# Kernel tuning notes

Hardware: AMD Instinct MI355X
Metric: run time of the kernel (lower is better)

Reference implementation:

```python
import jax, jax.numpy as jnp
import numpy as np

B, C, H, W = 8, 128, 48, 48
RED = 16  # SELayer reduction


def setup_inputs() -> dict:
    key = jax.random.key(0)
    ks = jax.random.split(key, 8)
    s = 0.05  # weight scale for numerical stability of softmax
    return {
        "x": jax.random.normal(ks[0], (B, C, H, W), jnp.float32),
        "Wq": jax.random.normal(ks[1], (C, C), jnp.float32) * s,
        "bq": jnp.zeros((C,), jnp.float32),
        "Wk": jax.random.normal(ks[2], (C, C), jnp.float32) * s,
        "bk": jnp.zeros((C,), jnp.float32),
        "Wv": jax.random.normal(ks[3], (C, C), jnp.float32) * s,
        "bv": jnp.zeros((C,), jnp.float32),
        "se_w1": jax.random.normal(ks[4], (C // RED, C), jnp.float32) * s,
        "se_w2": jax.random.normal(ks[5], (C, C // RED), jnp.float32) * s,
        "gamma": jax.random.normal(ks[6], (1,), jnp.float32),
    }


def reference(x, Wq, bq, Wk, bk, Wv, bv, se_w1, se_w2, gamma):
    b, c, h, w = x.shape
    n = h * w
    xf = x.reshape(b, c, n)  # (B, C, N)
    # 1x1 convs == per-pixel linear maps over channels
    q = jnp.einsum('oc,bcn->bon', Wq, xf) + bq[None, :, None]  # (B, C, N)
    k = jnp.einsum('oc,bcn->bon', Wk, xf) + bk[None, :, None]
    v = jnp.einsum('oc,bcn->bon', Wv, xf) + bv[None, :, None]
    # energy[b, i, j] = sum_c q[b, c, i] * k[b, c, j]  (unscaled, as in source)
    energy = jnp.einsum('bci,bcj->bij', q, k)  # (B, N, N)
    attn = jax.nn.softmax(energy, axis=-1)
    # out[b, c, i] = sum_j v[b, c, j] * attn[b, i, j]
    out = jnp.einsum('bcj,bij->bci', v, attn).reshape(b, c, h, w)
    # SELayer applied to the input x
    y = jnp.mean(x, axis=(2, 3))  # (B, C) global average pool
    y = jax.nn.relu(y @ se_w1.T)  # (B, C//RED)
    y = jax.nn.sigmoid(y @ se_w2.T)  # (B, C)
    x_se = x * y[:, :, None, None]
    return gamma[0] * out + x_se
```

## Files before the change

kernel.cpp:

```cpp
#include <hip/hip_runtime.h>

typedef _Float16 half8 __attribute__((ext_vector_type(8)));
typedef _Float16 half4 __attribute__((ext_vector_type(4)));
typedef float f32x4 __attribute__((ext_vector_type(4)));

#define BATCH 8
#define CH 128
#define NPIX 2304
#define SPLIT 4
#define JPER (NPIX / SPLIT)
#define BN (BATCH * NPIX)
#define LOG2E 1.44269504088896f

__device__ __forceinline__ f32x4 mfma32(half8 a, half8 b, f32x4 c) {
    return __builtin_amdgcn_mfma_f32_16x16x32_f16(a, b, c, 0, 0, 0);
}
__device__ __forceinline__ f32x4 mfma16(half4 a, half4 b, f32x4 c) {
    return __builtin_amdgcn_mfma_f32_16x16x16f16(a, b, c, 0, 0, 0);
}

__global__ __launch_bounds__(256) void k_prep(
        const float* __restrict__ x, const float* __restrict__ Wq,
        const float* __restrict__ Wk, const float* __restrict__ Wv,
        _Float16* __restrict__ Wh, float* __restrict__ y0) {
    const int bid = blockIdx.x;
    const int t = threadIdx.x;
    if (bid < 1024) {
        const int row = bid;
        const float4* p = (const float4*)(x + (size_t)row * NPIX);
        float s = 0.f;
        for (int tt = t; tt < NPIX / 4; tt += 256) {
            float4 v = p[tt];
            s += v.x + v.y + v.z + v.w;
        }
        for (int m = 1; m < 64; m <<= 1) s += __shfl_xor(s, m);
        __shared__ float ls[4];
        if ((t & 63) == 0) ls[t >> 6] = s;
        __syncthreads();
        if (t == 0) y0[row] = (ls[0] + ls[1] + ls[2] + ls[3]) * (1.0f / (float)NPIX);
    } else {
        int i = (bid - 1024) * 256 + t;
        const float* src = (i < 16384) ? Wq : ((i < 32768) ? Wk : Wv);
        Wh[i] = (_Float16)src[i & 16383];
    }
}

__global__ __launch_bounds__(256) void k_proj(
        const float* __restrict__ x, const _Float16* __restrict__ Wh,
        const float* __restrict__ bq, const float* __restrict__ bk, const float* __restrict__ bv,
        _Float16* __restrict__ qT, _Float16* __restrict__ kT, _Float16* __restrict__ vN,
        const float* __restrict__ y0, const float* __restrict__ se_w1,
        const float* __restrict__ se_w2, float* __restrict__ scale) {
    const int which = blockIdx.z;
    const int t = threadIdx.x;

    if (which == 3) {
        if (blockIdx.x != 0 || blockIdx.y != 0) return;
        __shared__ float ly[128];
        __shared__ float ly1[8];
        for (int b = 0; b < BATCH; ++b) {
            if (t < 128) ly[t] = y0[b * 128 + t];
            __syncthreads();
            if (t < 8) {
                float a = 0.f;
                for (int c = 0; c < 128; ++c) a += se_w1[t * 128 + c] * ly[c];
                ly1[t] = fmaxf(a, 0.f);
            }
            __syncthreads();
            if (t < 128) {
                float a = 0.f;
                for (int r = 0; r < 8; ++r) a += se_w2[t * 8 + r] * ly1[r];
                scale[b * 128 + t] = 1.f / (1.f + __expf(-a));
            }
            __syncthreads();
        }
        return;
    }

    const int n0 = blockIdx.x * 128;
    const int b = blockIdx.y;
    const float* bias = (which == 0) ? bq : ((which == 1) ? bk : bv);
    const _Float16* W = Wh + which * 16384;

    __shared__ __align__(16) _Float16 xt[128 * 128];

    {
        const float* xb = x + (size_t)b * CH * NPIX + n0;
        for (int rep = 0; rep < 16; ++rep) {
            int flat = rep * 256 + t;
            int c = flat >> 5;
            int n4 = (flat & 31) * 4;
            float4 v4 = *(const float4*)(xb + (size_t)c * NPIX + n4);
            int cc = c & 7, ck = c >> 3;
            xt[(n4 + 0) * 128 + ((ck ^ ((n4 + 0) & 7)) * 8) + cc] = (_Float16)v4.x;
            xt[(n4 + 1) * 128 + ((ck ^ ((n4 + 1) & 7)) * 8) + cc] = (_Float16)v4.y;
            xt[(n4 + 2) * 128 + ((ck ^ ((n4 + 2) & 7)) * 8) + cc] = (_Float16)v4.z;
            xt[(n4 + 3) * 128 + ((ck ^ ((n4 + 3) & 7)) * 8) + cc] = (_Float16)v4.w;
        }
    }
    __syncthreads();

    const int lane = t & 63, w = t >> 6;
    const int ln15 = lane & 15, quad = lane >> 4;

    f32x4 zero4 = {0.f, 0.f, 0.f, 0.f};
    f32x4 acc[8][2];
    for (int mt = 0; mt < 8; ++mt) { acc[mt][0] = zero4; acc[mt][1] = zero4; }

    for (int ks = 0; ks < 4; ++ks) {
        half8 bf[2];
        for (int nt = 0; nt < 2; ++nt) {
            int row = w * 32 + nt * 16 + ln15;
            int ch = ks * 4 + quad;
            bf[nt] = *(const half8*)(xt + row * 128 + ((ch ^ (row & 7)) * 8));
        }
        for (int mt = 0; mt < 8; ++mt) {
            half8 af = *(const half8*)(W + (mt * 16 + ln15) * 128 + ks * 32 + quad * 8);
            acc[mt][0] = mfma32(af, bf[0], acc[mt][0]);
            acc[mt][1] = mfma32(af, bf[1], acc[mt][1]);
        }
    }
    __syncthreads();

    if (which == 2) {
        for (int mt = 0; mt < 8; ++mt)
            for (int nt = 0; nt < 2; ++nt)
                for (int r = 0; r < 4; ++r) {
                    int c = mt * 16 + quad * 4 + r;
                    int nl = w * 32 + nt * 16 + ln15;
                    xt[c * 128 + (((nl >> 3) ^ (c & 7)) * 8) + (nl & 7)] =
                        (_Float16)(acc[mt][nt][r] + bias[c]);
                }
        __syncthreads();
        _Float16* vb = vN + (size_t)b * CH * NPIX + n0;
        for (int rep = 0; rep < 8; ++rep) {
            int c = rep * 16 + (t >> 4), ch = t & 15;
            *(half8*)(vb + (size_t)c * NPIX + ch * 8) =
                *(const half8*)(xt + c * 128 + ((ch ^ (c & 7)) * 8));
        }
    } else {
        for (int mt = 0; mt < 8; ++mt)
            for (int nt = 0; nt < 2; ++nt)
                for (int r = 0; r < 4; ++r) {
                    int c = mt * 16 + quad * 4 + r;
                    int nl = w * 32 + nt * 16 + ln15;
                    xt[nl * 128 + (((c >> 3) ^ (nl & 7)) * 8) + (c & 7)] =
                        (_Float16)(acc[mt][nt][r] + bias[c]);
                }
        __syncthreads();
        _Float16* dst = ((which == 0) ? qT : kT) + ((size_t)b * NPIX + n0) * CH;
        for (int rep = 0; rep < 8; ++rep) {
            int nl = rep * 16 + (t >> 4), ch = t & 15;
            *(half8*)(dst + nl * 128 + ch * 8) =
                *(const half8*)(xt + nl * 128 + ((ch ^ (nl & 7)) * 8));
        }
    }
}

__global__ __launch_bounds__(256, 4) void k_attn(
        const _Float16* __restrict__ qT, const _Float16* __restrict__ kT,
        const _Float16* __restrict__ vN,
        _Float16* __restrict__ o_part, float* __restrict__ g_m, float* __restrict__ g_l) {
    const int i0 = blockIdx.x * 64;
    const int b = blockIdx.y;
    const int split = blockIdx.z;
    const int t = threadIdx.x;
    const int lane = t & 63, w = t >> 6;
    const int ln15 = lane & 15, quad = lane >> 4;

    __shared__ __align__(16) _Float16 sh[16384];
    _Float16* k_s = sh;
    _Float16* v_s = sh + 8192;

    half8 qf[4];
    {
        const _Float16* qb = qT + ((size_t)b * NPIX + i0 + w * 16 + ln15) * CH + quad * 8;
        for (int kc = 0; kc < 4; ++kc) qf[kc] = *(const half8*)(qb + kc * 32);
    }

    f32x4 zero4 = {0.f, 0.f, 0.f, 0.f};
    f32x4 os[8];
    for (int ct = 0; ct < 8; ++ct) os[ct] = zero4;
    float m = -1e30f, l = 0.f;

    for (int it = 0; it < 9; ++it) {
        const int j0 = split * JPER + it * 64;
        __syncthreads();
        {
            const _Float16* kb = kT + ((size_t)b * NPIX + j0) * CH;
            for (int rep = 0; rep < 4; ++rep) {
                int row = rep * 16 + (t >> 4), ch = t & 15;
                *(half8*)(k_s + row * 128 + ((ch ^ (row & 7)) * 8)) =
                    *(const half8*)(kb + row * CH + ch * 8);
            }
        }
        {
            const _Float16* vb = vN + (size_t)b * CH * NPIX + j0;
            for (int rep = 0; rep < 4; ++rep) {
                int c = rep * 32 + (t >> 3), ch = t & 7;
                *(half8*)(v_s + c * 64 + ((ch ^ (c & 7)) * 8)) =
                    *(const half8*)(vb + (size_t)c * NPIX + ch * 8);
            }
        }
        __syncthreads();

        f32x4 s[4];
        for (int jt = 0; jt < 4; ++jt) s[jt] = zero4;
        for (int jt = 0; jt < 4; ++jt) {
            for (int kc = 0; kc < 4; ++kc) {
                int row = jt * 16 + ln15, ch = kc * 4 + quad;
                half8 kf = *(const half8*)(k_s + row * 128 + ((ch ^ (row & 7)) * 8));
                s[jt] = mfma32(kf, qf[kc], s[jt]);
            }
        }

        float mx = fmaxf(fmaxf(s[0][0], s[0][1]), fmaxf(s[0][2], s[0][3]));
        for (int jt = 1; jt < 4; ++jt)
            mx = fmaxf(mx, fmaxf(fmaxf(s[jt][0], s[jt][1]), fmaxf(s[jt][2], s[jt][3])));
        mx = fmaxf(mx, __shfl_xor(mx, 16));
        mx = fmaxf(mx, __shfl_xor(mx, 32));
        float mnew = fmaxf(m, mx);
        float alpha = exp2f((m - mnew) * LOG2E);
        m = mnew;
        float mbias = mnew * LOG2E;

        float sum = 0.f;
        half4 pf[4];
        for (int jt = 0; jt < 4; ++jt)
            for (int r = 0; r < 4; ++r) {
                float p = exp2f(fmaf(s[jt][r], LOG2E, -mbias));
                sum += p;
                pf[jt][r] = (_Float16)p;
            }
        sum += __shfl_xor(sum, 16);
        sum += __shfl_xor(sum, 32);
        l = l * alpha + sum;

        for (int ct = 0; ct < 8; ++ct) {
            os[ct][0] *= alpha; os[ct][1] *= alpha;
            os[ct][2] *= alpha; os[ct][3] *= alpha;
        }

        for (int ct = 0; ct < 8; ++ct) {
            int c = ct * 16 + ln15;
            for (int jt = 0; jt < 4; ++jt) {
                int chunk = jt * 2 + (quad >> 1);
                half4 vf = *(const half4*)(v_s + c * 64 + ((chunk ^ (c & 7)) * 8) + (quad & 1) * 4);
                os[ct] = mfma16(vf, pf[jt], os[ct]);
            }
        }
    }

    if (quad == 0) {
        int i = i0 + w * 16 + ln15;
        g_m[(size_t)(split * BATCH + b) * NPIX + i] = m;
        g_l[(size_t)(split * BATCH + b) * NPIX + i] = l;
    }
    __syncthreads();
    for (int ct = 0; ct < 8; ++ct)
        for (int r = 0; r < 4; ++r) {
            int c = ct * 16 + quad * 4 + r;
            int il = w * 16 + ln15;
            int chunk = (il >> 3);
            sh[c * 64 + ((chunk ^ (c & 7)) * 8) + (il & 7)] = (_Float16)os[ct][r];
        }
    __syncthreads();
    _Float16* op = o_part + (size_t)(split * BATCH + b) * CH * NPIX;
    for (int rep = 0; rep < 4; ++rep) {
        int c = rep * 32 + (t >> 3), ch = t & 7;
        *(half8*)(op + (size_t)c * NPIX + i0 + ch * 8) =
            *(const half8*)(sh + c * 64 + ((ch ^ (c & 7)) * 8));
    }
}

__global__ __launch_bounds__(256) void k_combine(
        const _Float16* __restrict__ o_part, const float* __restrict__ g_m,
        const float* __restrict__ g_l, const float* __restrict__ x,
        const float* __restrict__ scale, const float* __restrict__ gamma_p,
        float* __restrict__ out) {
    const int i0 = blockIdx.x * 64;
    const int b = blockIdx.y;
    const int t = threadIdx.x;
    __shared__ float wl[SPLIT][64];

    if (t < 64) {
        int i = i0 + t;
        float mm[SPLIT], llv[SPLIT];
        float M = -1e30f;
        for (int s = 0; s < SPLIT; ++s) {
            mm[s] = g_m[(size_t)(s * BATCH + b) * NPIX + i];
            llv[s] = g_l[(size_t)(s * BATCH + b) * NPIX + i];
            M = fmaxf(M, mm[s]);
        }
        float L = 0.f, e[SPLIT];
        for (int s = 0; s < SPLIT; ++s) {
            e[s] = exp2f((mm[s] - M) * LOG2E);
            L += e[s] * llv[s];
        }
        float inv = 1.f / L;
        for (int s = 0; s < SPLIT; ++s) wl[s][t] = e[s] * inv;
    }
    __syncthreads();

    const float g = gamma_p[0];
    for (int rep = 0; rep < 4; ++rep) {
        int c = rep * 32 + (t >> 3), i8 = (t & 7) * 8;
        size_t base = ((size_t)b * CH + c) * NPIX + i0 + i8;
        float acc[8] = {0.f, 0.f, 0.f, 0.f, 0.f, 0.f, 0.f, 0.f};
        for (int s = 0; s < SPLIT; ++s) {
            half8 o = *(const half8*)(o_part +
                ((size_t)(s * BATCH + b) * CH + c) * NPIX + i0 + i8);
            for (int e = 0; e < 8; ++e) acc[e] += wl[s][i8 + e] * (float)o[e];
        }
        float sc = scale[b * 128 + c];
        float4 x0 = *(const float4*)(x + base);
        float4 x1 = *(const float4*)(x + base + 4);
        float4 r0, r1;
        r0.x = g * acc[0] + x0.x * sc; r0.y = g * acc[1] + x0.y * sc;
        r0.z = g * acc[2] + x0.z * sc; r0.w = g * acc[3] + x0.w * sc;
        r1.x = g * acc[4] + x1.x * sc; r1.y = g * acc[5] + x1.y * sc;
        r1.z = g * acc[6] + x1.z * sc; r1.w = g * acc[7] + x1.w * sc;
        *(float4*)(out + base) = r0;
        *(float4*)(out + base + 4) = r1;
    }
}

extern "C" void kernel_launch(void* const* d_in, const int* in_sizes, int n_in,
                              void* d_out, int out_size, void* d_ws, size_t ws_size,
                              hipStream_t stream) {
    const float* x     = (const float*)d_in[0];
    const float* Wq    = (const float*)d_in[1];
    const float* bq    = (const float*)d_in[2];
    const float* Wk    = (const float*)d_in[3];
    const float* bk    = (const float*)d_in[4];
    const float* Wv    = (const float*)d_in[5];
    const float* bv    = (const float*)d_in[6];
    const float* se_w1 = (const float*)d_in[7];
    const float* se_w2 = (const float*)d_in[8];
    const float* gamma = (const float*)d_in[9];
    float* out = (float*)d_out;

    char* ws = (char*)d_ws;
    const size_t E = (size_t)BATCH * NPIX * CH;
    _Float16* qT = (_Float16*)(ws);
    _Float16* kT = (_Float16*)(ws + E * 2);
    _Float16* vN = (_Float16*)(ws + E * 4);
    _Float16* op = (_Float16*)(ws + E * 6);
    char* tail   = ws + E * 6 + (size_t)SPLIT * E * 2;
    _Float16* Wh = (_Float16*)(tail);
    float* g_m   = (float*)(tail + 98304);
    float* g_l   = (float*)(tail + 98304 + SPLIT * BN * 4);
    float* y0    = (float*)(tail + 98304 + 2 * SPLIT * BN * 4);
    float* scale = (float*)(tail + 98304 + 2 * SPLIT * BN * 4 + 4096);

    k_prep<<<1216, 256, 0, stream>>>(x, Wq, Wk, Wv, Wh, y0);
    k_proj<<<dim3(NPIX / 128, BATCH, 4), 256, 0, stream>>>(
        x, Wh, bq, bk, bv, qT, kT, vN, y0, se_w1, se_w2, scale);
    k_attn<<<dim3(NPIX / 64, BATCH, SPLIT), 256, 0, stream>>>(
        qT, kT, vN, op, g_m, g_l);
    k_combine<<<dim3(NPIX / 64, BATCH), 256, 0, stream>>>(
        op, g_m, g_l, x, scale, gamma, out);
}
```

Baseline: 163.4 us.

## Prefetch K/V tiles into registers, lazy softmax rescale, normalize partials before fp16 store

The attention kernel now loads the next K/V tile from global memory into registers while the current tile is being computed, then stores it to shared memory at the top of the next iteration. This replaces the load-then-barrier pattern and is meant to hide global load latency. It also skips the online-softmax rescale of the accumulators when the running max grows by less than a threshold, uses s_setprio around the MFMA sections, and normalizes partial outputs by l before the fp16 store, with the combine weights adjusted to match. The normalization should also reduce fp16 overflow risk when rescaling is skipped, at the cost of extra register pressure from the prefetch buffers.

```diff
diff --git a/kernel.cpp b/kernel.cpp
--- a/kernel.cpp
+++ b/kernel.cpp
@@ -178,34 +178,53 @@
         for (int kc = 0; kc < 4; ++kc) qf[kc] = *(const half8*)(qb + kc * 32);
     }
 
+    const int krow = t >> 4;
+    const int kch  = t & 15;
+    const int vco  = t >> 3;
+    const int vch  = t & 7;
+    const _Float16* kb0 = kT + ((size_t)b * NPIX) * CH;
+    const _Float16* vb0 = vN + (size_t)b * CH * NPIX;
+
+    half8 kr[4], vr[4];
+    {
+        const int j0 = split * JPER;
+        const _Float16* kb = kb0 + (size_t)(j0 + krow) * CH + kch * 8;
+        for (int r = 0; r < 4; ++r) kr[r] = *(const half8*)(kb + (size_t)(r * 16) * CH);
+        const _Float16* vb = vb0 + j0 + vch * 8;
+        for (int r = 0; r < 4; ++r) vr[r] = *(const half8*)(vb + (size_t)(r * 32 + vco) * NPIX);
+    }
+
     f32x4 zero4 = {0.f, 0.f, 0.f, 0.f};
     f32x4 os[8];
     for (int ct = 0; ct < 8; ++ct) os[ct] = zero4;
     float m = -1e30f, l = 0.f;
 
     for (int it = 0; it < 9; ++it) {
-        const int j0 = split * JPER + it * 64;
         __syncthreads();
+
         {
-            const _Float16* kb = kT + ((size_t)b * NPIX + j0) * CH;
-            for (int rep = 0; rep < 4; ++rep) {
-                int row = rep * 16 + (t >> 4), ch = t & 15;
-                *(half8*)(k_s + row * 128 + ((ch ^ (row & 7)) * 8)) =
-                    *(const half8*)(kb + row * CH + ch * 8);
-            }
-        }
-        {
-            const _Float16* vb = vN + (size_t)b * CH * NPIX + j0;
-            for (int rep = 0; rep < 4; ++rep) {
-                int c = rep * 32 + (t >> 3), ch = t & 7;
-                *(half8*)(v_s + c * 64 + ((ch ^ (c & 7)) * 8)) =
-                    *(const half8*)(vb + (size_t)c * NPIX + ch * 8);
-            }
-        }
-        __syncthreads();
+            for (int r = 0; r < 4; ++r) {
+                int row = r * 16 + krow;
+                *(half8*)(k_s + row * 128 + ((kch ^ (row & 7)) * 8)) = kr[r];
+            }
+            for (int r = 0; r < 4; ++r) {
+                int c = r * 32 + vco;
+                *(half8*)(v_s + c * 64 + ((vch ^ (c & 7)) * 8)) = vr[r];
+            }
+        }
+        if (it < 8) {
+            const int j0n = split * JPER + (it + 1) * 64;
+            const _Float16* kb = kb0 + (size_t)(j0n + krow) * CH + kch * 8;
+            for (int r = 0; r < 4; ++r) kr[r] = *(const half8*)(kb + (size_t)(r * 16) * CH);
+            const _Float16* vb = vb0 + j0n + vch * 8;
+            for (int r = 0; r < 4; ++r) vr[r] = *(const half8*)(vb + (size_t)(r * 32 + vco) * NPIX);
+        }
+        asm volatile("s_waitcnt lgkmcnt(0)" ::: "memory");
+        asm volatile("s_barrier" ::: "memory");
 
         f32x4 s[4];
         for (int jt = 0; jt < 4; ++jt) s[jt] = zero4;
+        __builtin_amdgcn_s_setprio(1);
         for (int jt = 0; jt < 4; ++jt) {
             for (int kc = 0; kc < 4; ++kc) {
                 int row = jt * 16 + ln15, ch = kc * 4 + quad;
@@ -213,16 +232,24 @@
                 s[jt] = mfma32(kf, qf[kc], s[jt]);
             }
         }
+        __builtin_amdgcn_s_setprio(0);
 
         float mx = fmaxf(fmaxf(s[0][0], s[0][1]), fmaxf(s[0][2], s[0][3]));
         for (int jt = 1; jt < 4; ++jt)
             mx = fmaxf(mx, fmaxf(fmaxf(s[jt][0], s[jt][1]), fmaxf(s[jt][2], s[jt][3])));
         mx = fmaxf(mx, __shfl_xor(mx, 16));
         mx = fmaxf(mx, __shfl_xor(mx, 32));
-        float mnew = fmaxf(m, mx);
-        float alpha = exp2f((m - mnew) * LOG2E);
-        m = mnew;
-        float mbias = mnew * LOG2E;
+        if (!__all(mx - m <= 8.0f)) {
+            float mnew = fmaxf(m, mx);
+            float alpha = exp2f((m - mnew) * LOG2E);
+            for (int ct = 0; ct < 8; ++ct) {
+                os[ct][0] *= alpha; os[ct][1] *= alpha;
+                os[ct][2] *= alpha; os[ct][3] *= alpha;
+            }
+            l *= alpha;
+            m = mnew;
+        }
+        float mbias = m * LOG2E;
 
         float sum = 0.f;
         half4 pf[4];
@@ -234,13 +261,9 @@
             }
         sum += __shfl_xor(sum, 16);
         sum += __shfl_xor(sum, 32);
-        l = l * alpha + sum;
-
-        for (int ct = 0; ct < 8; ++ct) {
-            os[ct][0] *= alpha; os[ct][1] *= alpha;
-            os[ct][2] *= alpha; os[ct][3] *= alpha;
-        }
-
+        l += sum;
+
+        __builtin_amdgcn_s_setprio(1);
         for (int ct = 0; ct < 8; ++ct) {
             int c = ct * 16 + ln15;
             for (int jt = 0; jt < 4; ++jt) {
@@ -249,6 +272,7 @@
                 os[ct] = mfma16(vf, pf[jt], os[ct]);
             }
         }
+        __builtin_amdgcn_s_setprio(0);
     }
 
     if (quad == 0) {
@@ -256,13 +280,14 @@
         g_m[(size_t)(split * BATCH + b) * NPIX + i] = m;
         g_l[(size_t)(split * BATCH + b) * NPIX + i] = l;
     }
+    const float linv = 1.0f / l;
     __syncthreads();
     for (int ct = 0; ct < 8; ++ct)
         for (int r = 0; r < 4; ++r) {
             int c = ct * 16 + quad * 4 + r;
             int il = w * 16 + ln15;
             int chunk = (il >> 3);
-            sh[c * 64 + ((chunk ^ (c & 7)) * 8) + (il & 7)] = (_Float16)os[ct][r];
+            sh[c * 64 + ((chunk ^ (c & 7)) * 8) + (il & 7)] = (_Float16)(os[ct][r] * linv);
         }
     __syncthreads();
     _Float16* op = o_part + (size_t)(split * BATCH + b) * CH * NPIX;
@@ -298,7 +323,7 @@
             L += e[s] * llv[s];
         }
         float inv = 1.f / L;
-        for (int s = 0; s < SPLIT; ++s) wl[s][t] = e[s] * inv;
+        for (int s = 0; s < SPLIT; ++s) wl[s][t] = e[s] * llv[s] * inv;
     }
     __syncthreads();
 
```

Result: slower. 172.2 us (+5.4%).
